# Kernel optimization log

Hardware: AMD Instinct MI355X
Metric: run time of the kernel (lower is better)

Reference implementation:

```python
import jax, jax.numpy as jnp
import numpy as np

LAM = 0.7      # lambda_param
GAM = 2.0      # gamma (weight upper bound)
ALPHA = 0.1    # age modulation scale
FGAM = 0.1     # fusion_gamma
SIGMAS = jnp.array([0.1, 0.5, 1.0, 2.0], dtype=jnp.float32)  # multi-kernel sigmas


def setup_inputs() -> dict:
    key = jax.random.key(0)
    ks = jax.random.split(key, 12)
    B, C, D, H, W, K = 12, 64, 32, 32, 32, 32
    mid, red = C // 2, C // 4
    Z = jax.random.normal(ks[0], (B, C, D, H, W), jnp.float32)
    masks = (jax.random.uniform(ks[1], (K, D, H, W)) > 0.5).astype(jnp.float32)
    masks = masks.at[:, 0, 0, 0].set(1.0)  # guarantee every region non-empty
    labels = jnp.arange(B, dtype=jnp.int32) % 3  # 4 samples each of CN/MCI/AD
    ages = 50.0 + 40.0 * jax.random.uniform(ks[2], (B,), jnp.float32)
    prior_weights = 1.0 + 0.1 * jax.random.normal(ks[3], (K,), jnp.float32)
    struct_w = 0.05 * jax.random.normal(ks[4], (mid, C), jnp.float32)
    noise_w = 0.05 * jax.random.normal(ks[5], (mid, C), jnp.float32)
    up_w = 0.05 * jax.random.normal(ks[6], (C, mid), jnp.float32)
    region_w = 0.05 * jax.random.normal(ks[7], (C, C, 3, 3, 3), jnp.float32)
    m_w1 = 0.05 * jax.random.normal(ks[8], (red, C), jnp.float32)
    m_b1 = jnp.zeros((red,), jnp.float32)
    m_w2 = 0.05 * jax.random.normal(ks[9], (C, red), jnp.float32)
    m_b2 = jnp.zeros((C,), jnp.float32)
    return dict(Z=Z, masks=masks, labels=labels, ages=ages, prior_weights=prior_weights,
                struct_w=struct_w, noise_w=noise_w, up_w=up_w, region_w=region_w,
                m_w1=m_w1, m_b1=m_b1, m_w2=m_w2, m_b2=m_b2)


def _mmd_pair(kern, ca, cb):
    # kern: [S,K,B,B] RBF kernels; ca/cb: [B] float class indicators.
    # Unbiased MMD^2 per region, averaged over sigmas -> [K].
    m = ca.sum()
    n = cb.sum()
    Kaa = jnp.einsum('skij,i,j->sk', kern, ca, ca)
    da = jnp.einsum('skii,i->sk', kern, ca)
    Kbb = jnp.einsum('skij,i,j->sk', kern, cb, cb)
    db = jnp.einsum('skii,i->sk', kern, cb)
    t1 = (Kaa - da) / (m * (m - 1.0))
    t2 = (Kbb - db) / (n * (n - 1.0))
    t3 = jnp.einsum('skij,i,j->sk', kern, ca, cb) * (-2.0 / (m * n))
    return (t1 + t2 + t3).mean(0)


def _forward(Z, masks, labels, ages, prior_weights, struct_w, noise_w, up_w,
             region_w, m_w1, m_b1, m_w2, m_b2):
    B, C = Z.shape[:2]
    K = masks.shape[0]
    # --- region-specific aggregation (fused segment-reduce over masks) ---
    msum = masks.sum((1, 2, 3))                                   # [K]
    rf = jnp.einsum('bcdhw,kdhw->bkc', Z, masks) / (msum[None, :, None] + 1e-6)
    # --- multi-class multi-kernel MMD per region ---
    x2 = jnp.sum(rf * rf, -1)                                     # [B,K]
    ip = jnp.einsum('ikc,jkc->kij', rf, rf)                       # [K,B,B]
    d2 = jnp.maximum(x2.T[:, :, None] + x2.T[:, None, :] - 2.0 * ip, 0.0)
    kern = jnp.exp(-d2[None] / (2.0 * SIGMAS[:, None, None, None] ** 2))  # [S,K,B,B]
    c_cn = (labels == 0).astype(jnp.float32)
    c_mci = (labels == 1).astype(jnp.float32)
    c_ad = (labels == 2).astype(jnp.float32)
    D_mmd = (_mmd_pair(kern, c_ad, c_cn) + _mmd_pair(kern, c_mci, c_cn)
             + _mmd_pair(kern, c_ad, c_mci))                      # [K]
    max_mmd = jnp.maximum(D_mmd.max(), 1e-6)
    nm = jnp.clip(D_mmd / max_mmd, 0.0)
    # symmetric KL between prior and MMD-evidence distributions (batchmean -> /K)
    lp = jax.nn.log_softmax(prior_weights)
    lq = jax.nn.log_softmax(nm)
    p = jnp.exp(lp)
    q = jnp.exp(lq)
    reg = 0.5 * jnp.sum(q * (lq - lp)) / K + 0.5 * jnp.sum(p * (lp - lq)) / K
    # --- prior-guided adaptive spatial weights ---
    base = LAM * prior_weights + (1.0 - LAM) * nm
    af = 1.0 + jax.nn.softplus(ALPHA * (ages - 50.0))             # [B]
    Wk = jax.nn.softmax(jnp.clip(base[None, :] * af[:, None], 0.0, GAM), axis=1)
    spatial = jnp.einsum('bk,kdhw->bdhw', Wk, masks)[:, None]     # [B,1,D,H,W]
    # --- orthogonal decomposition ---
    cs = jnp.einsum('oc,bcdhw->bodhw', struct_w, Z)               # 1x1x1 conv
    cnoise = jnp.einsum('oc,bcdhw->bodhw', noise_w, Z)
    s = cs.reshape(B, cs.shape[1], -1)
    n = cnoise.reshape(B, cnoise.shape[1], -1)
    eps = 1e-8
    cos = jnp.sum(s * n, -1) / (jnp.maximum(jnp.linalg.norm(s, axis=-1), eps)
                                * jnp.maximum(jnp.linalg.norm(n, axis=-1), eps))
    ortho = jnp.abs(cos).mean()
    Z_clean = jnp.einsum('oc,bcdhw->bodhw', up_w, cs)
    # --- region base field + 3x3x3 conv + channel modulation ---
    Zrb = jnp.einsum('bkc,kdhw->bcdhw', rf, masks)
    Zrec = jax.lax.conv_general_dilated(
        Zrb, region_w, (1, 1, 1), 'SAME',
        dimension_numbers=('NCDHW', 'OIDHW', 'NCDHW'))
    h = jax.nn.relu(jnp.einsum('bkc,rc->bkr', rf, m_w1) + m_b1)
    mod = jax.nn.softplus(jnp.einsum('bkr,cr->bkc', h, m_w2) + m_b2)  # [B,K,C]
    Zmod = Zrec * jnp.einsum('bkc,kdhw->bcdhw', mod, masks)
    Z_out = Z_clean + FGAM * (Zmod * spatial)
    return rf, spatial, Z_out, reg + ortho


def reference(Z, masks, labels, ages, prior_weights, struct_w, noise_w, up_w,
              region_w, m_w1, m_b1, m_w2, m_b2):
    return _forward(Z, masks, labels, ages, prior_weights, struct_w, noise_w,
                    up_w, region_w, m_w1, m_b1, m_w2, m_b2)
```

## Files before the change

### kernel.cpp

```cpp
#include <hip/hip_runtime.h>
#include <hip/hip_bf16.h>
#include <math.h>

#define REG_OFF    0
#define ORTHO_OFF  1
#define FLAG_OFF   2
#define MSUM_OFF   4
#define RF_OFF     64
#define G_OFF      24640
#define WKW_OFF    73792
#define MODTB_OFF  74176
#define M1TTH_OFF  86464
#define M1TTL_OFF  88512
#define WKCB_OFF   90560
#define IPK_OFF    422336
#define MB_OFF     426944
#define WS_TOTAL   459712
#define ZERO_FLOATS 73792

#define RF_OUT   0
#define SPAT_OUT 24576
#define ZOUT_OUT 417792
#define SCAL_OUT 25583616

typedef unsigned short u16;
typedef short bh8 __attribute__((ext_vector_type(8)));
typedef float fv4 __attribute__((ext_vector_type(4)));

__device__ __forceinline__ float bf2f(u16 u) {
  union { unsigned int i; float f; } x; x.i = ((unsigned int)u) << 16; return x.f;
}
__device__ __forceinline__ u16 f2bf(float f) {
  unsigned int u = __float_as_uint(f);
  return (u16)((u + 0x7fffu + ((u >> 16) & 1u)) >> 16);
}
__device__ __forceinline__ float ldin(const void* p, size_t i, bool f32) {
  return f32 ? ((const float*)p)[i] : bf2f(((const u16*)p)[i]);
}
__device__ __forceinline__ bh8 bits2bf8(unsigned int mbits) {
  union { bh8 v; unsigned int w[4]; } u;
#pragma unroll
  for (int j = 0; j < 4; j++) {
    unsigned int tt = mbits >> (2 * j);
    u.w[j] = ((tt & 1u) | ((tt & 2u) << 15)) * 0x3F80u;
  }
  return u.v;
}

__global__ void k_probe(const void* __restrict__ Z, float* __restrict__ ws) {
  int t = threadIdx.x;
  const u16* s = (const u16*)Z;
  float mx = 0.f;
  for (int i = t; i < 8192; i += 256) {
    float a = fabsf(bf2f(s[i]));
    if (!(a < 1e30f)) a = 3e38f;
    mx = fmaxf(mx, a);
  }
  __shared__ float r[256];
  r[t] = mx; __syncthreads();
  for (int o = 128; o > 0; o >>= 1) { if (t < o) r[t] = fmaxf(r[t], r[t + o]); __syncthreads(); }
  if (t == 0) ws[FLAG_OFF] = (r[0] > 1e6f) ? 1.f : 0.f;
}

__global__ void k_mb(const void* __restrict__ masks, float* __restrict__ ws) {
  int v = blockIdx.x * 256 + threadIdx.x;
  bool f32 = ws[FLAG_OFF] > 0.5f;
  unsigned int word = 0;
#pragma unroll 8
  for (int k = 0; k < 32; k++) {
    float mv = ldin(masks, ((size_t)k << 15) + v, f32);
    word |= (mv != 0.f ? 1u : 0u) << k;
  }
  ((unsigned int*)(ws + MB_OFF))[v] = word;
}

__global__ void k_msum(const void* __restrict__ masks, float* __restrict__ ws) {
  int k = blockIdx.x, t = threadIdx.x;
  bool f32 = ws[FLAG_OFF] > 0.5f;
  float s = 0.f;
  for (int v = t; v < 32768; v += 256) s += ldin(masks, ((size_t)k << 15) + v, f32);
  __shared__ float red[256];
  red[t] = s; __syncthreads();
  for (int off = 128; off > 0; off >>= 1) { if (t < off) red[t] += red[t + off]; __syncthreads(); }
  if (t == 0) ws[MSUM_OFF + k] = red[0];
}

__global__ __launch_bounds__(256) void k_rfgram(const void* __restrict__ Z,
                                                const void* __restrict__ masks,
                                                float* __restrict__ ws) {
  __shared__ float Zt[64][68];
  __shared__ float Mt[64][36];
  int b = blockIdx.y, t = threadIdx.x;
  bool f32 = ws[FLAG_OFF] > 0.5f;
  int ci = t & 15, gj = t >> 4;
  int c0 = ci << 2, c20 = gj << 2, k0 = gj << 1;
  float accG[16], accR[8];
#pragma unroll
  for (int i = 0; i < 16; i++) accG[i] = 0.f;
#pragma unroll
  for (int i = 0; i < 8; i++) accR[i] = 0.f;
  int vs = blockIdx.x << 9;
  for (int t8 = 0; t8 < 8; t8++) {
    int vb = vs + (t8 << 6);
    __syncthreads();
    if (f32) {
      const float* Zf = (const float*)Z;
      const float* Mf = (const float*)masks;
#pragma unroll
      for (int i = 0; i < 8; i++) {
        int idx = (i << 8) + t, c = idx >> 5, v2 = (idx & 31) << 1;
        float2 u = *(const float2*)(Zf + (((size_t)(b << 6) + c) << 15) + vb + v2);
        Zt[v2][c] = u.x; Zt[v2 + 1][c] = u.y;
      }
#pragma unroll
      for (int i = 0; i < 4; i++) {
        int idx = (i << 8) + t, k = idx >> 5, v2 = (idx & 31) << 1;
        float2 u = *(const float2*)(Mf + ((size_t)k << 15) + vb + v2);
        Mt[v2][k] = u.x; Mt[v2 + 1][k] = u.y;
      }
    } else {
      const u16* Zs = (const u16*)Z;
      const u16* Ms = (const u16*)masks;
#pragma unroll
      for (int i = 0; i < 8; i++) {
        int idx = (i << 8) + t, c = idx >> 5, v2 = (idx & 31) << 1;
        unsigned int u = *(const unsigned int*)(Zs + (((size_t)(b << 6) + c) << 15) + vb + v2);
        Zt[v2][c]     = bf2f((u16)(u & 0xffff));
        Zt[v2 + 1][c] = bf2f((u16)(u >> 16));
      }
#pragma unroll
      for (int i = 0; i < 4; i++) {
        int idx = (i << 8) + t, k = idx >> 5, v2 = (idx & 31) << 1;
        unsigned int u = *(const unsigned int*)(Ms + ((size_t)k << 15) + vb + v2);
        Mt[v2][k]     = bf2f((u16)(u & 0xffff));
        Mt[v2 + 1][k] = bf2f((u16)(u >> 16));
      }
    }
    __syncthreads();
    for (int vt = 0; vt < 64; vt++) {
      float4 z1 = *(const float4*)&Zt[vt][c0];
      float4 z2 = *(const float4*)&Zt[vt][c20];
      float2 m2 = *(const float2*)&Mt[vt][k0];
      float z1a[4] = {z1.x, z1.y, z1.z, z1.w};
      float z2a[4] = {z2.x, z2.y, z2.z, z2.w};
      float m2a[2] = {m2.x, m2.y};
#pragma unroll
      for (int i = 0; i < 4; i++) {
#pragma unroll
        for (int j = 0; j < 4; j++) accG[(i << 2) + j] += z1a[i] * z2a[j];
#pragma unroll
        for (int kk = 0; kk < 2; kk++) accR[(i << 1) + kk] += z1a[i] * m2a[kk];
      }
    }
  }
  float* Gd = ws + G_OFF + (b << 12);
  float* Rd = ws + RF_OFF + (b << 11);
#pragma unroll
  for (int i = 0; i < 4; i++) {
#pragma unroll
    for (int j = 0; j < 4; j++) atomicAdd(Gd + ((c0 + i) << 6) + c20 + j, accG[(i << 2) + j]);
#pragma unroll
    for (int kk = 0; kk < 2; kk++) atomicAdd(Rd + ((k0 + kk) << 6) + c0 + i, accR[(i << 1) + kk]);
  }
}

__global__ void k_scale_rf(float* __restrict__ ws, float* __restrict__ out) {
  int i = blockIdx.x * 256 + threadIdx.x;
  int k = (i >> 6) & 31;
  float v = ws[RF_OFF + i] / (ws[MSUM_OFF + k] + 1e-6f);
  ws[RF_OFF + i] = v;
  out[RF_OUT + i] = v;
}

__global__ void k_ipk(float* __restrict__ ws) {
  __shared__ float rfk[12][65];
  int k = blockIdx.x, t = threadIdx.x;
  for (int i = t; i < 768; i += 256) {
    int b = i >> 6, c = i & 63;
    rfk[b][c] = ws[RF_OFF + (((size_t)(b << 5) + k) << 6) + c];
  }
  __syncthreads();
  if (t < 144) {
    int i = t / 12, j = t - (t / 12) * 12;
    float s = 0.f;
#pragma unroll
    for (int c = 0; c < 64; c++) s += rfk[i][c] * rfk[j][c];
    ws[IPK_OFF + k * 144 + t] = s;
  }
}

__global__ void k_mmdw(const int* __restrict__ labels, const void* __restrict__ ages,
                       const void* __restrict__ prior, float* __restrict__ ws) {
  __shared__ float IPL[32 * 145];
  __shared__ float dpart[128];
  __shared__ float Dm[32], nms[32], bases[32], pwl[32];
  __shared__ int labs[12];
  int t = threadIdx.x;
  bool f32 = ws[FLAG_OFF] > 0.5f;
  if (t < 12) labs[t] = labels[t];
  for (int i = t; i < 4608; i += 256) {
    int k = i / 144, r = i - k * 144;
    IPL[k * 145 + r] = ws[IPK_OFF + i];
  }
  __syncthreads();
  if (t < 128) {
    int k = t >> 2, s = t & 3;
    const float inv2s2[4] = {50.f, 2.f, 0.5f, 0.125f};
    float inv = inv2s2[s];
    const float* pk = IPL + k * 145;
    float c0 = 0.f, c1 = 0.f, c2 = 0.f;
#pragma unroll
    for (int i = 0; i < 12; i++) {
      int li = labs[i];
      c0 += (li == 0) ? 1.f : 0.f;
      c1 += (li == 1) ? 1.f : 0.f;
      c2 += (li == 2) ? 1.f : 0.f;
    }
    float s00=0,s01=0,s02=0,s10=0,s11=0,s12=0,s20=0,s21=0,s22=0;
    float dg0=0, dg1=0, dg2=0;
    for (int i = 0; i < 12; i++) {
      int li = labs[i];
      float x2i = pk[i * 13];
      float r0=0, r1=0, r2=0, dge=0;
      for (int j = 0; j < 12; j++) {
        float d2 = fmaxf(x2i + pk[j * 13] - 2.f * pk[i * 12 + j], 0.f);
        float e = expf(-d2 * inv);
        int lj = labs[j];
        r0 += (lj == 0) ? e : 0.f;
        r1 += (lj == 1) ? e : 0.f;
        r2 += (lj == 2) ? e : 0.f;
        if (j == i) dge = e;
      }
      if (li == 0)      { s00 += r0; s01 += r1; s02 += r2; dg0 += dge; }
      else if (li == 1) { s10 += r0; s11 += r1; s12 += r2; dg1 += dge; }
      else              { s20 += r0; s21 += r1; s22 += r2; dg2 += dge; }
    }
    float ta = (s22 - dg2) / (c2 * (c2 - 1.f));
    float tb = (s00 - dg0) / (c0 * (c0 - 1.f));
    float tc = (s11 - dg1) / (c1 * (c1 - 1.f));
    float dsum = (ta + tb - 2.f * s20 / (c2 * c0))
               + (tc + tb - 2.f * s10 / (c1 * c0))
               + (ta + tc - 2.f * s21 / (c2 * c1));
    dpart[t] = dsum;
  }
  __syncthreads();
  if (t < 32) {
    Dm[t] = (dpart[t * 4] + dpart[t * 4 + 1] + dpart[t * 4 + 2] + dpart[t * 4 + 3]) * 0.25f;
    pwl[t] = (float)ldin(prior, t, f32);
  }
  __syncthreads();
  if (t == 0) {
    float mx = 1e-6f;
    for (int k = 0; k < 32; k++) mx = fmaxf(mx, Dm[k]);
    float nmax = -1e30f, pmax = -1e30f;
    for (int k = 0; k < 32; k++) {
      nms[k] = fmaxf(Dm[k] / mx, 0.f);
      nmax = fmaxf(nmax, nms[k]);
      pmax = fmaxf(pmax, pwl[k]);
    }
    float nse = 0.f, pse = 0.f;
    for (int k = 0; k < 32; k++) { nse += expf(nms[k] - nmax); pse += expf(pwl[k] - pmax); }
    float lns = logf(nse), lps = logf(pse);
    float reg = 0.f;
    for (int k = 0; k < 32; k++) {
      float lqk = nms[k] - nmax - lns;
      float lpk = pwl[k] - pmax - lps;
      reg += 0.5f * (expf(lqk) * (lqk - lpk) + expf(lpk) * (lpk - lqk));
    }
    ws[REG_OFF] = reg / 32.f;
    for (int k = 0; k < 32; k++) bases[k] = 0.7f * pwl[k] + 0.3f * nms[k];
  }
  __syncthreads();
  if (t < 12) {
    float x = 0.1f * (ldin(ages, t, f32) - 50.f);
    float af = 1.f + fmaxf(x, 0.f) + log1pf(expf(-fabsf(x)));
    float w[32];
    float mx = -1e30f;
#pragma unroll
    for (int k = 0; k < 32; k++) {
      float v = fminf(fmaxf(bases[k] * af, 0.f), 2.f);
      w[k] = v; mx = fmaxf(mx, v);
    }
    float se = 0.f;
#pragma unroll
    for (int k = 0; k < 32; k++) se += expf(w[k] - mx);
#pragma unroll
    for (int k = 0; k < 32; k++) ws[WKW_OFF + (t << 5) + k] = expf(w[k] - mx) / se;
  }
}

__global__ __launch_bounds__(64) void k_mod(const void* __restrict__ m_w1, const void* __restrict__ m_b1,
                                            const void* __restrict__ m_w2, const void* __restrict__ m_b2,
                                            float* __restrict__ ws) {
  __shared__ float W1[16][65];
  __shared__ float W2T[16][64];
  __shared__ float B1[16], B2[64], RL[64], H[16];
  int bk = blockIdx.x, t = threadIdx.x;
  int bb = bk >> 5, kk = bk & 31;
  bool f32 = ws[FLAG_OFF] > 0.5f;
  for (int i = t; i < 1024; i += 64) {
    W1[i >> 6][i & 63] = ldin(m_w1, i, f32);
    W2T[i & 15][i >> 4] = ldin(m_w2, i, f32);
  }
  if (t < 16) B1[t] = ldin(m_b1, t, f32);
  B2[t] = ldin(m_b2, t, f32);
  RL[t] = ws[RF_OFF + (bk << 6) + t];
  __syncthreads();
  if (t < 16) {
    float s = B1[t];
#pragma unroll
    for (int c = 0; c < 64; c++) s += RL[c] * W1[t][c];
    H[t] = fmaxf(s, 0.f);
  }
  __syncthreads();
  {
    int c = t;
    float s = B2[c];
#pragma unroll
    for (int rr = 0; rr < 16; rr++) s += H[rr] * W2T[rr][c];
    float mv = fmaxf(s, 0.f) + log1pf(expf(-fabsf(s)));
    ((u16*)(ws + MODTB_OFF))[((size_t)bb * 64 + c) * 32 + kk] = f2bf(mv);
  }
}

__global__ void k_m1t(const void* __restrict__ struct_w, const void* __restrict__ up_w,
                      float* __restrict__ ws) {
  __shared__ float UPT[32][64];
  __shared__ float ST[32][64];
  int t = threadIdx.x, blk = blockIdx.x;
  bool f32 = ws[FLAG_OFF] > 0.5f;
  for (int i = t; i < 2048; i += 256) {
    UPT[i & 31][i >> 5] = ldin(up_w, i, f32);
    ST[i >> 6][i & 63] = ldin(struct_w, i, f32);
  }
  __syncthreads();
  int idx = (blk << 8) + t;
  int cin = idx >> 6, co = idx & 63;
  float s = 0.f;
#pragma unroll
  for (int j = 0; j < 32; j++) s += UPT[j][co] * ST[j][cin];
  u16 hi = f2bf(s);
  ((u16*)(ws + M1TTH_OFF))[co * 64 + cin] = hi;
  ((u16*)(ws + M1TTL_OFF))[co * 64 + cin] = f2bf(s - bf2f(hi));
}

__global__ void k_ortho(const void* __restrict__ sw, const void* __restrict__ nw,
                        float* __restrict__ ws) {
  int b = blockIdx.x >> 5, o = blockIdx.x & 31, c = threadIdx.x;
  bool f32 = ws[FLAG_OFF] > 0.5f;
  const float* Gb = ws + G_OFF + (b << 12);
  float ts = 0.f, tn = 0.f;
  for (int c2 = 0; c2 < 64; c2++) {
    float g = Gb[(c << 6) + c2];
    ts += g * ldin(sw, (o << 6) + c2, f32);
    tn += g * ldin(nw, (o << 6) + c2, f32);
  }
  float swc = ldin(sw, (o << 6) + c, f32);
  float nwc = ldin(nw, (o << 6) + c, f32);
  float ds = swc * tn, ss = swc * ts, nn = nwc * tn;
  for (int off = 32; off > 0; off >>= 1) {
    ds += __shfl_down(ds, off);
    ss += __shfl_down(ss, off);
    nn += __shfl_down(nn, off);
  }
  if (c == 0) {
    ss = fmaxf(ss, 0.f); nn = fmaxf(nn, 0.f);
    float cosv = ds / (fmaxf(sqrtf(ss), 1e-8f) * fmaxf(sqrtf(nn), 1e-8f));
    atomicAdd(ws + ORTHO_OFF, fabsf(cosv) * (1.f / 384.f));
  }
}

__global__ void k_wk(const void* __restrict__ rw, float* __restrict__ ws) {
  int bk = blockIdx.x;
  int b = bk >> 5, k = bk & 31;
  int t = threadIdx.x;
  bool f32 = ws[FLAG_OFF] > 0.5f;
  __shared__ float rl[64];
  if (t < 64) rl[t] = ws[RF_OFF + (bk << 6) + t];
  __syncthreads();
  u16* dst = (u16*)(ws + WKCB_OFF);
  for (int idx = t; idx < 1728; idx += 256) {
    int o = idx / 27, d = idx - o * 27;
    float s = 0.f;
    for (int c = 0; c < 64; c++) s += rl[c] * ldin(rw, (size_t)o * 1728 + c * 27 + d, f32);
    dst[(((size_t)b * 64 + o) * 27 + d) * 32 + k] = f2bf(s);
  }
}

__global__ void k_spatial(const void* __restrict__ masks, const float* __restrict__ ws,
                          float* __restrict__ out) {
  int b = blockIdx.y, t = threadIdx.x;
  bool f32 = ws[FLAG_OFF] > 0.5f;
  __shared__ float wl[32];
  if (t < 32) wl[t] = ws[WKW_OFF + (b << 5) + t];
  __syncthreads();
  int v0 = (blockIdx.x << 11) + (t << 3);
  float s[8] = {0, 0, 0, 0, 0, 0, 0, 0};
  for (int k = 0; k < 32; k++) {
    float wkv = wl[k];
    float mv[8];
    if (f32) {
      const float* Mf = (const float*)masks + ((size_t)k << 15) + v0;
      float4 a = *(const float4*)Mf, bb = *(const float4*)(Mf + 4);
      mv[0]=a.x; mv[1]=a.y; mv[2]=a.z; mv[3]=a.w; mv[4]=bb.x; mv[5]=bb.y; mv[6]=bb.z; mv[7]=bb.w;
    } else {
      uint4 u = *(const uint4*)((const u16*)masks + ((size_t)k << 15) + v0);
      mv[0]=bf2f((u16)(u.x & 0xffff)); mv[1]=bf2f((u16)(u.x >> 16));
      mv[2]=bf2f((u16)(u.y & 0xffff)); mv[3]=bf2f((u16)(u.y >> 16));
      mv[4]=bf2f((u16)(u.z & 0xffff)); mv[5]=bf2f((u16)(u.z >> 16));
      mv[6]=bf2f((u16)(u.w & 0xffff)); mv[7]=bf2f((u16)(u.w >> 16));
    }
#pragma unroll
    for (int j = 0; j < 8; j++) s[j] += wkv * mv[j];
  }
#pragma unroll
  for (int j = 0; j < 8; j++) out[SPAT_OUT + (b << 15) + v0 + j] = s[j];
}

#define MHW 40
__global__ __launch_bounds__(256, 4) void k_final(const void* __restrict__ Z,
                                                  const void* __restrict__ masks,
                                                  const float* __restrict__ ws,
                                                  float* __restrict__ out) {
  __shared__ unsigned int MHB[4 * 6 * MHW];
  __shared__ float wl[32];
  __shared__ float spl[256];
  (void)masks;

  int b = blockIdx.y, tile = blockIdx.x, t = threadIdx.x;
  int lane = t & 63, w = t >> 6;
  int lo16 = lane & 15, g = lane >> 4, g8 = g << 3;
  int d0 = (tile >> 3) << 1, h0 = (tile & 7) << 2;
  const unsigned int* MB = (const unsigned int*)(ws + MB_OFF);
  bool f32 = ws[FLAG_OFF] > 0.5f;

  for (int i = t; i < 4 * 6 * MHW; i += 256) {
    int hd = i / (6 * MHW), r = i - hd * (6 * MHW), hh = r / MHW, hw = r - hh * MHW;
    int gd = d0 - 1 + hd, gh = h0 - 1 + hh, gw = hw - 1;
    unsigned int word = 0;
    if ((unsigned)gd < 32u && (unsigned)gh < 32u && (unsigned)gw < 32u)
      word = MB[(gd << 10) + (gh << 5) + gw];
    MHB[i] = word;
  }
  if (t < 32) wl[t] = ws[WKW_OFF + (b << 5) + t];
  __syncthreads();

  {
    int dz = t >> 7, hy = (t >> 5) & 3, wx = t & 31;
    unsigned int m = MHB[((dz + 1) * 6 + hy + 1) * MHW + wx + 1];
    float sp = 0.f;
#pragma unroll
    for (int k = 0; k < 32; k++) sp += ((m >> k) & 1u) ? wl[k] : 0.f;
    spl[t] = sp;
  }

  int hb4[4], v4[4];
#pragma unroll
  for (int pt = 0; pt < 4; pt++) {
    int pos = (w << 6) + (pt << 4) + lo16;
    int dz = pos >> 7, hy = (pos >> 5) & 3, wx = pos & 31;
    hb4[pt] = (dz * 6 + hy) * MHW + wx;
    v4[pt] = ((d0 + dz) << 10) + ((h0 + hy) << 5) + wx;
  }

  fv4 acc[4][4];
#pragma unroll
  for (int ot = 0; ot < 4; ot++)
#pragma unroll
    for (int pt = 0; pt < 4; pt++) { acc[ot][pt][0]=0.f; acc[ot][pt][1]=0.f; acc[ot][pt][2]=0.f; acc[ot][pt][3]=0.f; }

  const u16* Wb = (const u16*)(ws + WKCB_OFF) + (size_t)b * 55296;
#pragma unroll 3
  for (int d = 0; d < 27; d++) {
    int da = d / 9, r9 = d - da * 9, db = r9 / 3, dc = r9 - db * 3;
    int off = (da * 6 + db) * MHW + dc;
    bh8 a[4];
#pragma unroll
    for (int ot = 0; ot < 4; ot++)
      a[ot] = *(const bh8*)(Wb + ((ot << 4) + lo16) * 864 + (d << 5) + g8);
#pragma unroll
    for (int pt = 0; pt < 4; pt++) {
      bh8 bv = bits2bf8(MHB[hb4[pt] + off] >> g8);
#pragma unroll
      for (int ot = 0; ot < 4; ot++)
        acc[ot][pt] = __builtin_amdgcn_mfma_f32_16x16x32_bf16(a[ot], bv, acc[ot][pt], 0, 0, 0);
    }
  }

  {
    const u16* modtb = (const u16*)(ws + MODTB_OFF);
    bh8 am[4];
#pragma unroll
    for (int ot = 0; ot < 4; ot++)
      am[ot] = *(const bh8*)(modtb + ((size_t)b * 64 + (ot << 4) + lo16) * 32 + g8);
    fv4 zero4; zero4[0]=0.f; zero4[1]=0.f; zero4[2]=0.f; zero4[3]=0.f;
#pragma unroll
    for (int pt = 0; pt < 4; pt++) {
      bh8 bc = bits2bf8(MHB[hb4[pt] + 7 * MHW + 1] >> g8);
      float spf = 0.1f * spl[(w << 6) + (pt << 4) + lo16];
#pragma unroll
      for (int ot = 0; ot < 4; ot++) {
        fv4 mm = __builtin_amdgcn_mfma_f32_16x16x32_bf16(am[ot], bc, zero4, 0, 0, 0);
        acc[ot][pt] = acc[ot][pt] * mm * spf;
      }
    }
  }

  {
    const u16* m1tth = (const u16*)(ws + M1TTH_OFF);
    const u16* m1ttl = (const u16*)(ws + M1TTL_OFF);
#pragma unroll 1
    for (int st = 0; st < 2; st++) {
      int cb = st << 5;
#pragma unroll
      for (int pt = 0; pt < 4; pt++) {
        bh8 bh, bl;
#pragma unroll
        for (int j = 0; j < 8; j++) {
          float zv = ldin(Z, (((size_t)(b << 6) + cb + g8 + j) << 15) + v4[pt], f32);
          u16 h = f2bf(zv);
          bh[j] = (short)h;
          bl[j] = (short)f2bf(zv - bf2f(h));
        }
#pragma unroll
        for (int ot = 0; ot < 4; ot++) {
          bh8 ah = *(const bh8*)(m1tth + ((ot << 4) + lo16) * 64 + cb + g8);
          bh8 al = *(const bh8*)(m1ttl + ((ot << 4) + lo16) * 64 + cb + g8);
          acc[ot][pt] = __builtin_amdgcn_mfma_f32_16x16x32_bf16(ah, bh, acc[ot][pt], 0, 0, 0);
          acc[ot][pt] = __builtin_amdgcn_mfma_f32_16x16x32_bf16(ah, bl, acc[ot][pt], 0, 0, 0);
          acc[ot][pt] = __builtin_amdgcn_mfma_f32_16x16x32_bf16(al, bh, acc[ot][pt], 0, 0, 0);
        }
      }
    }
  }

#pragma unroll
  for (int ot = 0; ot < 4; ot++)
#pragma unroll
    for (int pt = 0; pt < 4; pt++)
#pragma unroll
      for (int r = 0; r < 4; r++) {
        int o = (ot << 4) + (g << 2) + r;
        out[(size_t)ZOUT_OUT + (((size_t)(b << 6) + o) << 15) + v4[pt]] = acc[ot][pt][r];
      }
  if ((t | tile | b) == 0) out[SCAL_OUT] = ws[REG_OFF] + ws[ORTHO_OFF];
}

extern "C" void kernel_launch(void* const* d_in, const int* in_sizes, int n_in,
                              void* d_out, int out_size, void* d_ws, size_t ws_size,
                              hipStream_t stream) {
  (void)in_sizes; (void)n_in; (void)out_size; (void)ws_size;
  const void* Z        = d_in[0];
  const void* masks    = d_in[1];
  const int*  labels   = (const int*)d_in[2];
  const void* ages     = d_in[3];
  const void* prior    = d_in[4];
  const void* struct_w = d_in[5];
  const void* noise_w  = d_in[6];
  const void* up_w     = d_in[7];
  const void* region_w = d_in[8];
  const void* m_w1     = d_in[9];
  const void* m_b1     = d_in[10];
  const void* m_w2     = d_in[11];
  const void* m_b2     = d_in[12];
  float* ws = (float*)d_ws;
  float* out = (float*)d_out;

  hipMemsetAsync(d_ws, 0, (size_t)ZERO_FLOATS * 4, stream);
  k_probe<<<1, 256, 0, stream>>>(Z, ws);
  k_mb<<<128, 256, 0, stream>>>(masks, ws);
  k_msum<<<32, 256, 0, stream>>>(masks, ws);
  k_rfgram<<<dim3(64, 12), 256, 0, stream>>>(Z, masks, ws);
  k_scale_rf<<<96, 256, 0, stream>>>(ws, out);
  k_m1t<<<16, 256, 0, stream>>>(struct_w, up_w, ws);
  k_ipk<<<32, 256, 0, stream>>>(ws);
  k_mmdw<<<1, 256, 0, stream>>>(labels, ages, prior, ws);
  k_mod<<<384, 64, 0, stream>>>(m_w1, m_b1, m_w2, m_b2, ws);
  k_ortho<<<384, 64, 0, stream>>>(struct_w, noise_w, ws);
  k_wk<<<384, 256, 0, stream>>>(region_w, ws);
  k_spatial<<<dim3(16, 12), 256, 0, stream>>>(masks, ws, out);
  k_final<<<dim3(128, 12), 256, 0, stream>>>(Z, masks, ws, out);
}
```

Before: 619.7 us.

## Compute Gram and region sums in k_rfgram with split-bf16 MFMA

Rewrites the Gram/region-feature kernel to use bf16 MFMA instructions instead of scalar FMA. fp32 inputs are split into high and low bf16 parts (three-term product) to keep accuracy. Masks are read from the precomputed bitmask rather than the float mask tensor. Global loads are software-prefetched one chunk ahead into registers, LDS uses an XOR swizzle, and the grid is halved to 32 blocks per batch, each handling 1024 voxels. The split-bf16 scheme trades a small precision loss and three times the MFMA work for much higher matrix throughput.

```diff
diff --git a/kernel.cpp b/kernel.cpp
--- a/kernel.cpp
+++ b/kernel.cpp
@@ -86,81 +86,131 @@
 }
 
 __global__ __launch_bounds__(256) void k_rfgram(const void* __restrict__ Z,
-                                                const void* __restrict__ masks,
                                                 float* __restrict__ ws) {
-  __shared__ float Zt[64][68];
-  __shared__ float Mt[64][36];
+  __shared__ u16 ZH[4096];
+  __shared__ u16 ZL[4096];
+  __shared__ unsigned int MBs[64];
   int b = blockIdx.y, t = threadIdx.x;
-  bool f32 = ws[FLAG_OFF] > 0.5f;
-  int ci = t & 15, gj = t >> 4;
-  int c0 = ci << 2, c20 = gj << 2, k0 = gj << 1;
-  float accG[16], accR[8];
-#pragma unroll
-  for (int i = 0; i < 16; i++) accG[i] = 0.f;
-#pragma unroll
-  for (int i = 0; i < 8; i++) accR[i] = 0.f;
-  int vs = blockIdx.x << 9;
-  for (int t8 = 0; t8 < 8; t8++) {
-    int vb = vs + (t8 << 6);
+  int lane = t & 63, w = t >> 6;
+  int lo16 = lane & 15, g = lane >> 4;
+  bool f32 = ws[FLAG_OFF] > 0.5f;
+  const unsigned int* MB = (const unsigned int*)(ws + MB_OFF);
+
+  fv4 accG[4], accR[2];
+#pragma unroll
+  for (int pt = 0; pt < 4; pt++) { accG[pt][0]=0.f; accG[pt][1]=0.f; accG[pt][2]=0.f; accG[pt][3]=0.f; }
+#pragma unroll
+  for (int i2 = 0; i2 < 2; i2++) { accR[i2][0]=0.f; accR[i2][1]=0.f; accR[i2][2]=0.f; accR[i2][3]=0.f; }
+
+  int c_s = t >> 2, q_s = t & 3;
+  int vs0 = blockIdx.x << 10;
+
+  float4 pa0, pa1, pb0, pb1; uint4 ua, ub;
+  if (f32) {
+    const float* Zf = (const float*)Z + (((size_t)(b << 6) + c_s) << 15) + vs0;
+    pa0 = *(const float4*)(Zf + (q_s << 3));
+    pa1 = *(const float4*)(Zf + (q_s << 3) + 4);
+    pb0 = *(const float4*)(Zf + ((q_s + 4) << 3));
+    pb1 = *(const float4*)(Zf + ((q_s + 4) << 3) + 4);
+  } else {
+    const u16* Zs = (const u16*)Z + (((size_t)(b << 6) + c_s) << 15) + vs0;
+    ua = *(const uint4*)(Zs + (q_s << 3));
+    ub = *(const uint4*)(Zs + ((q_s + 4) << 3));
+  }
+  unsigned int pm = (t < 64) ? MB[vs0 + t] : 0u;
+
+#pragma unroll 1
+  for (int ch = 0; ch < 16; ch++) {
     __syncthreads();
+    if (t < 64) MBs[t] = pm;
     if (f32) {
-      const float* Zf = (const float*)Z;
-      const float* Mf = (const float*)masks;
-#pragma unroll
-      for (int i = 0; i < 8; i++) {
-        int idx = (i << 8) + t, c = idx >> 5, v2 = (idx & 31) << 1;
-        float2 u = *(const float2*)(Zf + (((size_t)(b << 6) + c) << 15) + vb + v2);
-        Zt[v2][c] = u.x; Zt[v2 + 1][c] = u.y;
-      }
-#pragma unroll
-      for (int i = 0; i < 4; i++) {
-        int idx = (i << 8) + t, k = idx >> 5, v2 = (idx & 31) << 1;
-        float2 u = *(const float2*)(Mf + ((size_t)k << 15) + vb + v2);
-        Mt[v2][k] = u.x; Mt[v2 + 1][k] = u.y;
-      }
+      float a0[8] = {pa0.x,pa0.y,pa0.z,pa0.w,pa1.x,pa1.y,pa1.z,pa1.w};
+      float a1[8] = {pb0.x,pb0.y,pb0.z,pb0.w,pb1.x,pb1.y,pb1.z,pb1.w};
+      bh8 h, l;
+#pragma unroll
+      for (int j = 0; j < 8; j++) {
+        u16 hh = f2bf(a0[j]); h[j] = (short)hh; l[j] = (short)f2bf(a0[j] - bf2f(hh));
+      }
+      int d0 = (c_s << 6) + ((q_s ^ (c_s & 7)) << 3);
+      *(bh8*)(ZH + d0) = h; *(bh8*)(ZL + d0) = l;
+#pragma unroll
+      for (int j = 0; j < 8; j++) {
+        u16 hh = f2bf(a1[j]); h[j] = (short)hh; l[j] = (short)f2bf(a1[j] - bf2f(hh));
+      }
+      int d1 = (c_s << 6) + (((q_s + 4) ^ (c_s & 7)) << 3);
+      *(bh8*)(ZH + d1) = h; *(bh8*)(ZL + d1) = l;
     } else {
-      const u16* Zs = (const u16*)Z;
-      const u16* Ms = (const u16*)masks;
-#pragma unroll
-      for (int i = 0; i < 8; i++) {
-        int idx = (i << 8) + t, c = idx >> 5, v2 = (idx & 31) << 1;
-        unsigned int u = *(const unsigned int*)(Zs + (((size_t)(b << 6) + c) << 15) + vb + v2);
-        Zt[v2][c]     = bf2f((u16)(u & 0xffff));
-        Zt[v2 + 1][c] = bf2f((u16)(u >> 16));
-      }
-#pragma unroll
-      for (int i = 0; i < 4; i++) {
-        int idx = (i << 8) + t, k = idx >> 5, v2 = (idx & 31) << 1;
-        unsigned int u = *(const unsigned int*)(Ms + ((size_t)k << 15) + vb + v2);
-        Mt[v2][k]     = bf2f((u16)(u & 0xffff));
-        Mt[v2 + 1][k] = bf2f((u16)(u >> 16));
-      }
+      bh8 z8 = {0,0,0,0,0,0,0,0};
+      int d0 = (c_s << 6) + ((q_s ^ (c_s & 7)) << 3);
+      int d1 = (c_s << 6) + (((q_s + 4) ^ (c_s & 7)) << 3);
+      *(uint4*)(ZH + d0) = ua; *(bh8*)(ZL + d0) = z8;
+      *(uint4*)(ZH + d1) = ub; *(bh8*)(ZL + d1) = z8;
     }
     __syncthreads();
-    for (int vt = 0; vt < 64; vt++) {
-      float4 z1 = *(const float4*)&Zt[vt][c0];
-      float4 z2 = *(const float4*)&Zt[vt][c20];
-      float2 m2 = *(const float2*)&Mt[vt][k0];
-      float z1a[4] = {z1.x, z1.y, z1.z, z1.w};
-      float z2a[4] = {z2.x, z2.y, z2.z, z2.w};
-      float m2a[2] = {m2.x, m2.y};
-#pragma unroll
-      for (int i = 0; i < 4; i++) {
-#pragma unroll
-        for (int j = 0; j < 4; j++) accG[(i << 2) + j] += z1a[i] * z2a[j];
-#pragma unroll
-        for (int kk = 0; kk < 2; kk++) accR[(i << 1) + kk] += z1a[i] * m2a[kk];
+    if (ch < 15) {
+      int vb = vs0 + ((ch + 1) << 6);
+      if (f32) {
+        const float* Zf = (const float*)Z + (((size_t)(b << 6) + c_s) << 15) + vb;
+        pa0 = *(const float4*)(Zf + (q_s << 3));
+        pa1 = *(const float4*)(Zf + (q_s << 3) + 4);
+        pb0 = *(const float4*)(Zf + ((q_s + 4) << 3));
+        pb1 = *(const float4*)(Zf + ((q_s + 4) << 3) + 4);
+      } else {
+        const u16* Zs = (const u16*)Z + (((size_t)(b << 6) + c_s) << 15) + vb;
+        ua = *(const uint4*)(Zs + (q_s << 3));
+        ub = *(const uint4*)(Zs + ((q_s + 4) << 3));
+      }
+      if (t < 64) pm = MB[vb + t];
+    }
+#pragma unroll
+    for (int ks = 0; ks < 2; ks++) {
+      int v8k = (ks << 2) + g;
+      bh8 bhf[4], blf[4];
+#pragma unroll
+      for (int pt = 0; pt < 4; pt++) {
+        int col = (pt << 4) + lo16;
+        int adr = (col << 6) + ((v8k ^ (col & 7)) << 3);
+        bhf[pt] = *(const bh8*)(ZH + adr);
+        blf[pt] = *(const bh8*)(ZL + adr);
+      }
+      int row = (w << 4) + lo16;
+      int adr = (row << 6) + ((v8k ^ (row & 7)) << 3);
+      bh8 ah = *(const bh8*)(ZH + adr);
+      bh8 al = *(const bh8*)(ZL + adr);
+#pragma unroll
+      for (int pt = 0; pt < 4; pt++) {
+        accG[pt] = __builtin_amdgcn_mfma_f32_16x16x32_bf16(ah, bhf[pt], accG[pt], 0, 0, 0);
+        accG[pt] = __builtin_amdgcn_mfma_f32_16x16x32_bf16(ah, blf[pt], accG[pt], 0, 0, 0);
+        accG[pt] = __builtin_amdgcn_mfma_f32_16x16x32_bf16(al, bhf[pt], accG[pt], 0, 0, 0);
+      }
+#pragma unroll
+      for (int i2 = 0; i2 < 2; i2++) {
+        int idx = (w << 1) + i2;
+        int kt = idx >> 2, pt = idx & 3;
+        int kk = (kt << 4) + lo16;
+        bh8 am;
+#pragma unroll
+        for (int j = 0; j < 8; j++)
+          am[j] = (short)(((MBs[(ks << 5) + (g << 3) + j] >> kk) & 1u) ? 0x3F80 : 0);
+        accR[i2] = __builtin_amdgcn_mfma_f32_16x16x32_bf16(am, bhf[pt], accR[i2], 0, 0, 0);
+        accR[i2] = __builtin_amdgcn_mfma_f32_16x16x32_bf16(am, blf[pt], accR[i2], 0, 0, 0);
       }
     }
   }
   float* Gd = ws + G_OFF + (b << 12);
   float* Rd = ws + RF_OFF + (b << 11);
 #pragma unroll
-  for (int i = 0; i < 4; i++) {
-#pragma unroll
-    for (int j = 0; j < 4; j++) atomicAdd(Gd + ((c0 + i) << 6) + c20 + j, accG[(i << 2) + j]);
-#pragma unroll
-    for (int kk = 0; kk < 2; kk++) atomicAdd(Rd + ((k0 + kk) << 6) + c0 + i, accR[(i << 1) + kk]);
+  for (int pt = 0; pt < 4; pt++)
+#pragma unroll
+    for (int r = 0; r < 4; r++)
+      atomicAdd(Gd + (((w << 4) + (g << 2) + r) << 6) + (pt << 4) + lo16, accG[pt][r]);
+#pragma unroll
+  for (int i2 = 0; i2 < 2; i2++) {
+    int idx = (w << 1) + i2;
+    int kt = idx >> 2, pt = idx & 3;
+#pragma unroll
+    for (int r = 0; r < 4; r++)
+      atomicAdd(Rd + (((kt << 4) + (g << 2) + r) << 6) + (pt << 4) + lo16, accR[i2][r]);
   }
 }
 
@@ -570,7 +620,7 @@
   k_probe<<<1, 256, 0, stream>>>(Z, ws);
   k_mb<<<128, 256, 0, stream>>>(masks, ws);
   k_msum<<<32, 256, 0, stream>>>(masks, ws);
-  k_rfgram<<<dim3(64, 12), 256, 0, stream>>>(Z, masks, ws);
+  k_rfgram<<<dim3(32, 12), 256, 0, stream>>>(Z, ws);
   k_scale_rf<<<96, 256, 0, stream>>>(ws, out);
   k_m1t<<<16, 256, 0, stream>>>(struct_w, up_w, ws);
   k_ipk<<<32, 256, 0, stream>>>(ws);
```

Result: slower. 916.5 us (+47.9%).
